# Optimization experiments

Measured on AMD Instinct MI355X. Metric: run time of the kernel, lower is better.

## Reference

```python
import jax, jax.numpy as jnp
import numpy as np

TAW = 0.02

def setup_inputs() -> dict:
    key = jax.random.key(0)
    k1, k2 = jax.random.split(key)
    query = jax.random.normal(k1, (8, 2048, 1024), dtype=jnp.float32)
    memory = jax.random.normal(k2, (8, 2048, 1024), dtype=jnp.float32)
    return {"query": query, "memory": memory}

def reference(query, memory):
    # scores: [B, Lq, Lkv]
    scores = jnp.einsum('bqd,bkd->bqk', query, memory) / TAW
    probs = jax.nn.softmax(scores, axis=-1)
    # out: [B, Lq, D]
    return jnp.einsum('bqk,bkd->bqd', probs, memory)
```

## Files before the change

kernel.cpp:

```cpp
#include <hip/hip_runtime.h>
#include <math.h>


typedef __bf16 bf16x8 __attribute__((ext_vector_type(8)));
typedef float  f32x4  __attribute__((ext_vector_type(4)));
typedef float  f32x16 __attribute__((ext_vector_type(16)));

constexpr int   B_    = 8;
constexpr int   L_    = 2048;
constexpr int   D_    = 1024;
constexpr float SCALE  = 50.0f;
constexpr float MARGIN = 1.2f;
constexpr int   BQ    = 64;
constexpr int   RCAP  = 64;

constexpr size_t WS_T_ELEMS = (size_t)8 * 64 * 2048 * 16;
constexpr size_t WS_NEED    = 2 * WS_T_ELEMS * 2;

static __device__ __forceinline__ unsigned short f2bf(float x) {
    unsigned u = __builtin_bit_cast(unsigned, x);
    u += 0x7FFFu + ((u >> 16) & 1u);
    return (unsigned short)(u >> 16);
}

__global__ __launch_bounds__(256) void convert_k(
    const float* __restrict__ Q, const float* __restrict__ M,
    __bf16* __restrict__ ws)
{
    __shared__ unsigned short lds[64][72];

    const int t   = blockIdx.y;
    const int x   = blockIdx.x;
    const int d0  = x & 15;
    const int r0  = (x >> 4) & 31;
    const int b   = x >> 9;
    const int tid = threadIdx.x;

    const float* src = (t ? M : Q)
                     + ((size_t)b * L_ + (size_t)r0 * 64) * D_ + d0 * 64;

    {
        const int row = tid >> 4;
        const int c4  = tid & 15;
        #pragma unroll
        for (int a = 0; a < 4; ++a) {
            const int rr = a * 16 + row;
            float4 v = *(const float4*)(src + (size_t)rr * D_ + c4 * 4);
            union { unsigned short h[4]; uint2 u; } o;
            o.h[0] = f2bf(v.x); o.h[1] = f2bf(v.y);
            o.h[2] = f2bf(v.z); o.h[3] = f2bf(v.w);
            *(uint2*)&lds[rr][c4 * 4] = o.u;
        }
    }
    __syncthreads();

    {
        const int r    = tid & 63;
        const int d4   = tid >> 6;
        const int dblk = d0 * 4 + d4;
        __bf16* dst = ws + ((size_t)t * 8 + b) * (64ull * 2048 * 16)
                         + ((size_t)dblk * 2048 + (size_t)r0 * 64 + r) * 16;
        uint4 u0 = *(const uint4*)&lds[r][d4 * 16];
        uint4 u1 = *(const uint4*)&lds[r][d4 * 16 + 8];
        ((uint4*)dst)[0] = u0;
        ((uint4*)dst)[1] = u1;
    }
}

__global__ __launch_bounds__(512, 2) void attn_main(
    const float* __restrict__ Q, const float* __restrict__ M,
    const __bf16* __restrict__ ws, float* __restrict__ Out)
{
    __shared__ float wmax[8][BQ];
    __shared__ float rm_s[BQ], thr_s[BQ];
    __shared__ int   rowcnt[BQ];
    __shared__ int   rowlist[BQ][RCAP];
    __shared__ float rowval[BQ][RCAP];

    const int b    = blockIdx.x & 7;
    const int qt   = blockIdx.x >> 3;
    const int q0   = qt * BQ;
    const int tid  = threadIdx.x;
    const int w    = tid >> 6;
    const int lane = tid & 63;
    const int ln31 = lane & 31;
    const int h2   = lane >> 5;

    const __bf16* qws = ws + (size_t)b * (64ull * 2048 * 16);
    const __bf16* mws = ws + ((size_t)8 + b) * (64ull * 2048 * 16);
    const float*  Qb  = Q + ((size_t)b * L_ + q0) * D_;
    const float*  Mb  = M + (size_t)b * L_ * D_;

    if (tid < BQ) { rm_s[tid] = -INFINITY; rowcnt[tid] = 0; }
    __syncthreads();

    constexpr size_t DSTR = 2048 * 16;

    #pragma unroll 1
    for (int kt = 0; kt < 2; ++kt) {
        const int nb = kt * 1024 + w * 128;

        f32x16 acc[2][4];
        #pragma unroll
        for (int i = 0; i < 2; ++i)
            #pragma unroll
            for (int j = 0; j < 4; ++j)
                #pragma unroll
                for (int e = 0; e < 16; ++e) acc[i][j][e] = 0.f;

        const __bf16* qpb = qws + ((size_t)(q0 + ln31)) * 16 + h2 * 8;
        const __bf16* mpb = mws + ((size_t)(nb + ln31)) * 16 + h2 * 8;

        bf16x8 aA0, aA1, bA0, bA1, bA2, bA3;
        bf16x8 aB0, aB1, bB0, bB1, bB2, bB3;

#define LOADSET(s, dblk_) do {                                             \
        const __bf16* qp_##s = qpb + (size_t)(dblk_) * DSTR;               \
        const __bf16* mp_##s = mpb + (size_t)(dblk_) * DSTR;               \
        a##s##0 = *(const bf16x8*)(qp_##s);                                \
        a##s##1 = *(const bf16x8*)(qp_##s + 32 * 16);                      \
        b##s##0 = *(const bf16x8*)(mp_##s);                                \
        b##s##1 = *(const bf16x8*)(mp_##s + 32 * 16);                      \
        b##s##2 = *(const bf16x8*)(mp_##s + 64 * 16);                      \
        b##s##3 = *(const bf16x8*)(mp_##s + 96 * 16);                      \
    } while (0)

#define MFMASET(s) do {                                                    \
        acc[0][0] = __builtin_amdgcn_mfma_f32_32x32x16_bf16(               \
            a##s##0, b##s##0, acc[0][0], 0, 0, 0);                         \
        acc[0][1] = __builtin_amdgcn_mfma_f32_32x32x16_bf16(               \
            a##s##0, b##s##1, acc[0][1], 0, 0, 0);                         \
        acc[0][2] = __builtin_amdgcn_mfma_f32_32x32x16_bf16(               \
            a##s##0, b##s##2, acc[0][2], 0, 0, 0);                         \
        acc[0][3] = __builtin_amdgcn_mfma_f32_32x32x16_bf16(               \
            a##s##0, b##s##3, acc[0][3], 0, 0, 0);                         \
        acc[1][0] = __builtin_amdgcn_mfma_f32_32x32x16_bf16(               \
            a##s##1, b##s##0, acc[1][0], 0, 0, 0);                         \
        acc[1][1] = __builtin_amdgcn_mfma_f32_32x32x16_bf16(               \
            a##s##1, b##s##1, acc[1][1], 0, 0, 0);                         \
        acc[1][2] = __builtin_amdgcn_mfma_f32_32x32x16_bf16(               \
            a##s##1, b##s##2, acc[1][2], 0, 0, 0);                         \
        acc[1][3] = __builtin_amdgcn_mfma_f32_32x32x16_bf16(               \
            a##s##1, b##s##3, acc[1][3], 0, 0, 0);                         \
    } while (0)

        LOADSET(A, 0);
        #pragma unroll 1
        for (int d = 0; d < 62; d += 2) {
            LOADSET(B, d + 1);
            MFMASET(A);
            LOADSET(A, d + 2);
            MFMASET(B);
        }
        LOADSET(B, 63);
        MFMASET(A);
        MFMASET(B);

#undef LOADSET
#undef MFMASET

        float lm[2][16];
        #pragma unroll
        for (int i = 0; i < 2; ++i)
            #pragma unroll
            for (int g = 0; g < 16; ++g)
                lm[i][g] = fmaxf(fmaxf(acc[i][0][g], acc[i][1][g]),
                                 fmaxf(acc[i][2][g], acc[i][3][g]));
        #pragma unroll
        for (int off = 1; off <= 16; off <<= 1)
            #pragma unroll
            for (int i = 0; i < 2; ++i)
                #pragma unroll
                for (int g = 0; g < 16; ++g)
                    lm[i][g] = fmaxf(lm[i][g], __shfl_xor(lm[i][g], off, 64));
        if (ln31 == 0) {
            #pragma unroll
            for (int i = 0; i < 2; ++i)
                #pragma unroll
                for (int g = 0; g < 16; ++g)
                    wmax[w][i * 32 + (g & 3) + 8 * (g >> 2) + 4 * h2] = lm[i][g];
        }
        __syncthreads();
        if (tid < BQ) {
            float m = wmax[0][tid];
            #pragma unroll
            for (int ww = 1; ww < 8; ++ww) m = fmaxf(m, wmax[ww][tid]);
            m = fmaxf(m, rm_s[tid]);
            rm_s[tid] = m;
            thr_s[tid] = m - MARGIN;
        }
        __syncthreads();

        #pragma unroll
        for (int i = 0; i < 2; ++i)
            #pragma unroll
            for (int g = 0; g < 16; ++g) {
                const int rl = i * 32 + (g & 3) + 8 * (g >> 2) + 4 * h2;
                const float thr = thr_s[rl];
                #pragma unroll
                for (int j = 0; j < 4; ++j)
                    if (acc[i][j][g] > thr) {
                        int t = atomicAdd(&rowcnt[rl], 1);
                        if (t < RCAP) {
                            rowlist[rl][t] = nb + j * 32 + ln31;
                            rowval[rl][t]  = acc[i][j][g];
                        }
                    }
            }
    }
    __syncthreads();

    #pragma unroll 1
    for (int r = w; r < BQ; r += 8) {
        const int c = min(rowcnt[r], RCAP);
        const float thrf = rm_s[r] - MARGIN;
        #pragma unroll 1
        for (int t = 0; t < c; ++t) {
            const float av = rowval[r][t];
            if (av > thrf) {
                const int k = rowlist[r][t];
                const f32x4* qp = (const f32x4*)(Qb + (size_t)r * D_);
                const f32x4* mp = (const f32x4*)(Mb + (size_t)k * D_);
                float dot = 0.f;
                #pragma unroll
                for (int c4 = 0; c4 < 4; ++c4) {
                    f32x4 x = qp[lane + 64 * c4];
                    f32x4 y = mp[lane + 64 * c4];
                    dot += x[0]*y[0] + x[1]*y[1] + x[2]*y[2] + x[3]*y[3];
                }
                #pragma unroll
                for (int off = 32; off >= 1; off >>= 1)
                    dot += __shfl_xor(dot, off, 64);
                if (lane == 0) rowval[r][t] = dot;
            } else if (lane == 0) rowval[r][t] = -1e30f;
        }
    }
    __syncthreads();

    #pragma unroll 1
    for (int r = w; r < BQ; r += 8) {
        const int c = min(rowcnt[r], RCAP);
        float mstar = -1e30f;
        for (int t = 0; t < c; ++t) mstar = fmaxf(mstar, rowval[r][t]);
        float denom = 0.f;
        f32x4 o[4];
        #pragma unroll
        for (int c4 = 0; c4 < 4; ++c4) o[c4] = (f32x4){0.f, 0.f, 0.f, 0.f};
        #pragma unroll 1
        for (int t = 0; t < c; ++t) {
            const float wgt = __expf(SCALE * (rowval[r][t] - mstar));
            if (wgt > 1e-22f) {
                denom += wgt;
                const f32x4* mp = (const f32x4*)(Mb + (size_t)rowlist[r][t] * D_);
                #pragma unroll
                for (int c4 = 0; c4 < 4; ++c4)
                    o[c4] += mp[lane + 64 * c4] * wgt;
            }
        }
        const float inv = 1.f / denom;
        f32x4* op = (f32x4*)(Out + ((size_t)b * L_ + q0 + r) * D_);
        #pragma unroll
        for (int c4 = 0; c4 < 4; ++c4) op[lane + 64 * c4] = o[c4] * inv;
    }
}

constexpr int   FB_BKV  = 256;
constexpr int   FB_NKT  = L_ / FB_BKV;
constexpr int   FB_BD   = 32;
constexpr int   FB_NDC  = D_ / FB_BD;
constexpr int   FB_STR  = FB_BD + 8;
constexpr int   FB_CAP  = 2048;

__global__ __launch_bounds__(256) void attn_fb(
    const float* __restrict__ Q, const float* __restrict__ M,
    float* __restrict__ Out)
{
    __shared__ __bf16 qs[BQ * FB_STR];
    __shared__ __bf16 ms[FB_BKV * FB_STR];
    __shared__ float  wmax[4][BQ];
    __shared__ float  rowmax_s[BQ];
    __shared__ int    cnt_s;
    __shared__ int    list_s[FB_CAP];
    __shared__ float  elist_s[FB_CAP];

    const int b    = blockIdx.x & 7;
    const int qt   = blockIdx.x >> 3;
    const int q0   = qt * BQ;
    const int tid  = threadIdx.x;
    const int w    = tid >> 6;
    const int lane = tid & 63;
    const int ln15 = lane & 15;
    const int quad = lane >> 4;

    const float* Qb = Q + ((size_t)b * L_ + q0) * D_;
    const float* Mb = M + (size_t)b * L_ * D_;

    float rm[4][4];
    #pragma unroll
    for (int i = 0; i < 4; ++i)
        #pragma unroll
        for (int r = 0; r < 4; ++r) rm[i][r] = -INFINITY;

    #pragma unroll 1
    for (int pass = 0; pass < 2; ++pass) {
        #pragma unroll 1
        for (int kt = 0; kt < FB_NKT; ++kt) {
            f32x4 acc[4][4];
            #pragma unroll
            for (int i = 0; i < 4; ++i)
                #pragma unroll
                for (int j = 0; j < 4; ++j)
                    acc[i][j] = (f32x4){0.f, 0.f, 0.f, 0.f};
            const float* Mt = Mb + (size_t)(kt * FB_BKV) * D_;
            #pragma unroll 1
            for (int dc = 0; dc < FB_NDC; ++dc) {
                const int d0 = dc * FB_BD;
                __syncthreads();
                #pragma unroll
                for (int i = 0; i < 2; ++i) {
                    int f4 = tid + i * 256, row = f4 >> 3, c = f4 & 7;
                    float4 v = *(const float4*)(Qb + row * D_ + d0 + c * 4);
                    union { unsigned short h[4]; uint2 u; } t;
                    t.h[0] = f2bf(v.x); t.h[1] = f2bf(v.y);
                    t.h[2] = f2bf(v.z); t.h[3] = f2bf(v.w);
                    *(uint2*)(qs + row * FB_STR + c * 4) = t.u;
                }
                #pragma unroll
                for (int i = 0; i < 8; ++i) {
                    int f4 = tid + i * 256, row = f4 >> 3, c = f4 & 7;
                    float4 v = *(const float4*)(Mt + row * D_ + d0 + c * 4);
                    union { unsigned short h[4]; uint2 u; } t;
                    t.h[0] = f2bf(v.x); t.h[1] = f2bf(v.y);
                    t.h[2] = f2bf(v.z); t.h[3] = f2bf(v.w);
                    *(uint2*)(ms + row * FB_STR + c * 4) = t.u;
                }
                __syncthreads();
                bf16x8 afr[4], bfr[4];
                #pragma unroll
                for (int i = 0; i < 4; ++i)
                    afr[i] = *(const bf16x8*)(qs + (i * 16 + ln15) * FB_STR + quad * 8);
                #pragma unroll
                for (int j = 0; j < 4; ++j)
                    bfr[j] = *(const bf16x8*)(ms + (w * 64 + j * 16 + ln15) * FB_STR + quad * 8);
                #pragma unroll
                for (int i = 0; i < 4; ++i)
                    #pragma unroll
                    for (int j = 0; j < 4; ++j)
                        acc[i][j] = __builtin_amdgcn_mfma_f32_16x16x32_bf16(
                            afr[i], bfr[j], acc[i][j], 0, 0, 0);
            }
            if (pass == 0) {
                #pragma unroll
                for (int i = 0; i < 4; ++i)
                    #pragma unroll
                    for (int r = 0; r < 4; ++r) {
                        float m0 = fmaxf(fmaxf(acc[i][0][r], acc[i][1][r]),
                                         fmaxf(acc[i][2][r], acc[i][3][r]));
                        rm[i][r] = fmaxf(rm[i][r], m0);
                    }
            } else {
                #pragma unroll
                for (int i = 0; i < 4; ++i)
                    #pragma unroll
                    for (int j = 0; j < 4; ++j)
                        #pragma unroll
                        for (int r = 0; r < 4; ++r)
                            if (acc[i][j][r] > rm[i][r]) {
                                int idx = atomicAdd(&cnt_s, 1);
                                if (idx < FB_CAP)
                                    list_s[idx] = ((i * 16 + quad * 4 + r) << 16) |
                                                  (kt * FB_BKV + w * 64 + j * 16 + ln15);
                            }
            }
        }
        if (pass == 0) {
            #pragma unroll
            for (int i = 0; i < 4; ++i)
                #pragma unroll
                for (int r = 0; r < 4; ++r) {
                    float v = rm[i][r];
                    v = fmaxf(v, __shfl_xor(v, 1, 64));
                    v = fmaxf(v, __shfl_xor(v, 2, 64));
                    v = fmaxf(v, __shfl_xor(v, 4, 64));
                    v = fmaxf(v, __shfl_xor(v, 8, 64));
                    rm[i][r] = v;
                }
            if (ln15 == 0) {
                #pragma unroll
                for (int i = 0; i < 4; ++i)
                    #pragma unroll
                    for (int r = 0; r < 4; ++r)
                        wmax[w][i * 16 + quad * 4 + r] = rm[i][r];
            }
            __syncthreads();
            if (tid < BQ)
                rowmax_s[tid] = fmaxf(fmaxf(wmax[0][tid], wmax[1][tid]),
                                      fmaxf(wmax[2][tid], wmax[3][tid]));
            if (tid == 0) cnt_s = 0;
            __syncthreads();
            #pragma unroll
            for (int i = 0; i < 4; ++i)
                #pragma unroll
                for (int r = 0; r < 4; ++r)
                    rm[i][r] = rowmax_s[i * 16 + quad * 4 + r] - MARGIN;
        }
    }
    __syncthreads();
    const int n = min(cnt_s, FB_CAP);
    #pragma unroll 1
    for (int s = w; s < n; s += 4) {
        int e = list_s[s];
        int q = e >> 16, k = e & 0xFFFF;
        const float4* qp = (const float4*)(Qb + q * D_);
        const float4* mp = (const float4*)(Mb + (size_t)k * D_);
        float dot = 0.f;
        #pragma unroll
        for (int c = 0; c < 4; ++c) {
            float4 x = qp[lane + 64 * c];
            float4 y = mp[lane + 64 * c];
            dot += x.x * y.x + x.y * y.y + x.z * y.z + x.w * y.w;
        }
        #pragma unroll
        for (int off = 32; off >= 1; off >>= 1)
            dot += __shfl_xor(dot, off, 64);
        if (lane == 0) elist_s[s] = dot;
    }
    __syncthreads();
    #pragma unroll 1
    for (int r = w; r < BQ; r += 4) {
        float mstar = -INFINITY;
        for (int s = 0; s < n; ++s)
            if ((list_s[s] >> 16) == r) mstar = fmaxf(mstar, elist_s[s]);
        float denom = 0.f;
        f32x4 o[4];
        #pragma unroll
        for (int c = 0; c < 4; ++c) o[c] = (f32x4){0.f, 0.f, 0.f, 0.f};
        for (int s = 0; s < n; ++s) {
            if ((list_s[s] >> 16) != r) continue;
            float wgt = __expf(SCALE * (elist_s[s] - mstar));
            denom += wgt;
            const f32x4* mp = (const f32x4*)(Mb + (size_t)(list_s[s] & 0xFFFF) * D_);
            #pragma unroll
            for (int c = 0; c < 4; ++c) o[c] += mp[lane + 64 * c] * wgt;
        }
        const float inv = 1.f / denom;
        f32x4* op = (f32x4*)(Out + ((size_t)b * L_ + q0 + r) * D_);
        #pragma unroll
        for (int c = 0; c < 4; ++c) op[lane + 64 * c] = o[c] * inv;
    }
}

extern "C" void kernel_launch(void* const* d_in, const int* in_sizes, int n_in,
                              void* d_out, int out_size, void* d_ws, size_t ws_size,
                              hipStream_t stream)
{
    const float* Q = (const float*)d_in[0];
    const float* M = (const float*)d_in[1];
    float* Out = (float*)d_out;

    if (ws_size >= WS_NEED) {
        convert_k<<<dim3(4096, 2), 256, 0, stream>>>(Q, M, (__bf16*)d_ws);
        attn_main<<<dim3(256), 512, 0, stream>>>(Q, M, (const __bf16*)d_ws, Out);
    } else {
        attn_fb<<<dim3(256), 256, 0, stream>>>(Q, M, Out);
    }
}
```

Baseline: 278.5 us.

## Shrink per-wave key tile to 64 and deepen load pipeline to four stages

Each wave now covers 64 key columns per pass instead of 128, and the pass count over the key dimension rises from 2 to 4. The MFMA inner loop becomes a 4-deep rotating register prefetch with wrap-around indexing, so loads are issued further ahead of use. This cuts accumulator registers, which may raise occupancy and hide memory latency better. In exchange the Q tile is reloaded twice as often, there are more block-level syncs and threshold passes, and the wrap-around prefetch issues a few redundant loads.

New measurement: 328.4 us. +17.9%, slower.

```diff
diff --git a/kernel.cpp b/kernel.cpp
--- a/kernel.cpp
+++ b/kernel.cpp
@@ -96,23 +96,26 @@
 
     constexpr size_t DSTR = 2048 * 16;
 
-    #pragma unroll 1
-    for (int kt = 0; kt < 2; ++kt) {
-        const int nb = kt * 1024 + w * 128;
-
-        f32x16 acc[2][4];
+    const __bf16* qpb = qws + ((size_t)(q0 + ln31)) * 16 + h2 * 8;
+
+    #pragma unroll 1
+    for (int kt = 0; kt < 4; ++kt) {
+        const int nb = kt * 512 + w * 64;
+
+        f32x16 acc[2][2];
         #pragma unroll
         for (int i = 0; i < 2; ++i)
             #pragma unroll
-            for (int j = 0; j < 4; ++j)
+            for (int j = 0; j < 2; ++j)
                 #pragma unroll
                 for (int e = 0; e < 16; ++e) acc[i][j][e] = 0.f;
 
-        const __bf16* qpb = qws + ((size_t)(q0 + ln31)) * 16 + h2 * 8;
         const __bf16* mpb = mws + ((size_t)(nb + ln31)) * 16 + h2 * 8;
 
-        bf16x8 aA0, aA1, bA0, bA1, bA2, bA3;
-        bf16x8 aB0, aB1, bB0, bB1, bB2, bB3;
+        bf16x8 aA0, aA1, bA0, bA1;
+        bf16x8 aB0, aB1, bB0, bB1;
+        bf16x8 aC0, aC1, bC0, bC1;
+        bf16x8 aD0, aD1, bD0, bD1;
 
 #define LOADSET(s, dblk_) do {                                             \
         const __bf16* qp_##s = qpb + (size_t)(dblk_) * DSTR;               \
@@ -121,8 +124,6 @@
         a##s##1 = *(const bf16x8*)(qp_##s + 32 * 16);                      \
         b##s##0 = *(const bf16x8*)(mp_##s);                                \
         b##s##1 = *(const bf16x8*)(mp_##s + 32 * 16);                      \
-        b##s##2 = *(const bf16x8*)(mp_##s + 64 * 16);                      \
-        b##s##3 = *(const bf16x8*)(mp_##s + 96 * 16);                      \
     } while (0)
 
 #define MFMASET(s) do {                                                    \
@@ -130,31 +131,26 @@
             a##s##0, b##s##0, acc[0][0], 0, 0, 0);                         \
         acc[0][1] = __builtin_amdgcn_mfma_f32_32x32x16_bf16(               \
             a##s##0, b##s##1, acc[0][1], 0, 0, 0);                         \
-        acc[0][2] = __builtin_amdgcn_mfma_f32_32x32x16_bf16(               \
-            a##s##0, b##s##2, acc[0][2], 0, 0, 0);                         \
-        acc[0][3] = __builtin_amdgcn_mfma_f32_32x32x16_bf16(               \
-            a##s##0, b##s##3, acc[0][3], 0, 0, 0);                         \
         acc[1][0] = __builtin_amdgcn_mfma_f32_32x32x16_bf16(               \
             a##s##1, b##s##0, acc[1][0], 0, 0, 0);                         \
         acc[1][1] = __builtin_amdgcn_mfma_f32_32x32x16_bf16(               \
             a##s##1, b##s##1, acc[1][1], 0, 0, 0);                         \
-        acc[1][2] = __builtin_amdgcn_mfma_f32_32x32x16_bf16(               \
-            a##s##1, b##s##2, acc[1][2], 0, 0, 0);                         \
-        acc[1][3] = __builtin_amdgcn_mfma_f32_32x32x16_bf16(               \
-            a##s##1, b##s##3, acc[1][3], 0, 0, 0);                         \
     } while (0)
 
         LOADSET(A, 0);
+        LOADSET(B, 1);
+        LOADSET(C, 2);
         #pragma unroll 1
-        for (int d = 0; d < 62; d += 2) {
-            LOADSET(B, d + 1);
+        for (int d = 0; d < 64; d += 4) {
+            LOADSET(D, (d + 3) & 63);
             MFMASET(A);
-            LOADSET(A, d + 2);
+            LOADSET(A, (d + 4) & 63);
             MFMASET(B);
-        }
-        LOADSET(B, 63);
-        MFMASET(A);
-        MFMASET(B);
+            LOADSET(B, (d + 5) & 63);
+            MFMASET(C);
+            LOADSET(C, (d + 6) & 63);
+            MFMASET(D);
+        }
 
 #undef LOADSET
 #undef MFMASET
@@ -164,8 +160,7 @@
         for (int i = 0; i < 2; ++i)
             #pragma unroll
             for (int g = 0; g < 16; ++g)
-                lm[i][g] = fmaxf(fmaxf(acc[i][0][g], acc[i][1][g]),
-                                 fmaxf(acc[i][2][g], acc[i][3][g]));
+                lm[i][g] = fmaxf(acc[i][0][g], acc[i][1][g]);
         #pragma unroll
         for (int off = 1; off <= 16; off <<= 1)
             #pragma unroll
@@ -198,7 +193,7 @@
                 const int rl = i * 32 + (g & 3) + 8 * (g >> 2) + 4 * h2;
                 const float thr = thr_s[rl];
                 #pragma unroll
-                for (int j = 0; j < 4; ++j)
+                for (int j = 0; j < 2; ++j)
                     if (acc[i][j][g] > thr) {
                         int t = atomicAdd(&rowcnt[rl], 1);
                         if (t < RCAP) {
```

## Stage memory tiles into LDS via async global_load_lds with triple buffering

Applied to the files above, without the earlier changes.

The score GEMM loop now streams the memory operand through a per-wave triple-buffered LDS staging area using direct global-to-LDS loads, then reads fragments from LDS. Query fragments still come straight from global memory. Explicit vmcnt/lgkmcnt waits schedule loads three chunks ahead of the MFMAs, to hide global latency better than the previous register double-buffering. It adds about 104 KB of LDS per block, which may lower occupancy below the two-blocks launch bound. The hand-written waitcnt counts are fragile, and a dummy LDS buffer absorbs the out-of-range tail loads.

Result: slower. 288.2 us (+3.5%).

```diff
diff --git a/kernel.cpp b/kernel.cpp
--- a/kernel.cpp
+++ b/kernel.cpp
@@ -53,7 +53,6 @@
         }
     }
     __syncthreads();
-
     {
         const int r    = tid & 63;
         const int d4   = tid >> 6;
@@ -67,6 +66,64 @@
     }
 }
 
+constexpr size_t DSTR = 2048 * 16;
+constexpr int    CHW  = 2048;
+
+#define GLL16(srcp, dstp)                                                   \
+    __builtin_amdgcn_global_load_lds(                                       \
+        (const __attribute__((address_space(1))) void*)(srcp),              \
+        (__attribute__((address_space(3))) void*)(dstp), 16, 0, 0)
+
+#define STAGE4(srcp, dstp) do {                                             \
+        GLL16((srcp),         (dstp));                                      \
+        GLL16((srcp) +  512,  (dstp) +  512);                               \
+        GLL16((srcp) + 1024,  (dstp) + 1024);                               \
+        GLL16((srcp) + 1536,  (dstp) + 1536);                               \
+    } while (0)
+
+#define DSREAD4(s, rp) do {                                                 \
+        s##0 = *(const bf16x8*)((rp));                                      \
+        s##1 = *(const bf16x8*)((rp) +  512);                               \
+        s##2 = *(const bf16x8*)((rp) + 1024);                               \
+        s##3 = *(const bf16x8*)((rp) + 1536);                               \
+    } while (0)
+
+#define MFMASET(bs, qs) do {                                                \
+        acc[0][0] = __builtin_amdgcn_mfma_f32_32x32x16_bf16(                \
+            qs##0, bs##0, acc[0][0], 0, 0, 0);                              \
+        acc[0][1] = __builtin_amdgcn_mfma_f32_32x32x16_bf16(                \
+            qs##0, bs##1, acc[0][1], 0, 0, 0);                              \
+        acc[0][2] = __builtin_amdgcn_mfma_f32_32x32x16_bf16(                \
+            qs##0, bs##2, acc[0][2], 0, 0, 0);                              \
+        acc[0][3] = __builtin_amdgcn_mfma_f32_32x32x16_bf16(                \
+            qs##0, bs##3, acc[0][3], 0, 0, 0);                              \
+        acc[1][0] = __builtin_amdgcn_mfma_f32_32x32x16_bf16(                \
+            qs##1, bs##0, acc[1][0], 0, 0, 0);                              \
+        acc[1][1] = __builtin_amdgcn_mfma_f32_32x32x16_bf16(                \
+            qs##1, bs##1, acc[1][1], 0, 0, 0);                              \
+        acc[1][2] = __builtin_amdgcn_mfma_f32_32x32x16_bf16(                \
+            qs##1, bs##2, acc[1][2], 0, 0, 0);                              \
+        acc[1][3] = __builtin_amdgcn_mfma_f32_32x32x16_bf16(                \
+            qs##1, bs##3, acc[1][3], 0, 0, 0);                              \
+    } while (0)
+
+#define PHASE(dd, bc, qc, bn, qn) do {                                      \
+        asm volatile("s_waitcnt vmcnt(6)" ::: "memory");                    \
+        { const __bf16* rp = buf0 + (size_t)(((dd) + 1) % 3) * CHW + roff;  \
+          DSREAD4(bn, rp); }                                                \
+        asm volatile("s_waitcnt lgkmcnt(4)" ::: "memory");                  \
+        { const int c1 = (dd) + 1 <= 63 ? (dd) + 1 : 63;                    \
+          const __bf16* qp = qbase + (size_t)c1 * DSTR;                     \
+          qn##0 = *(const bf16x8*)(qp);                                     \
+          qn##1 = *(const bf16x8*)(qp + 512); }                             \
+        { const int c3 = (dd) + 3;                                          \
+          const __bf16* sp = mlane + (size_t)(c3 <= 63 ? c3 : 63) * DSTR;   \
+          __bf16* sd = (c3 <= 63) ? (buf0 + (size_t)(c3 % 3) * CHW)         \
+                                  : dummy_s;                                \
+          STAGE4(sp, sd); }                                                 \
+        MFMASET(bc, qc);                                                    \
+    } while (0)
+
 __global__ __launch_bounds__(512, 2) void attn_main(
     const float* __restrict__ Q, const float* __restrict__ M,
     const __bf16* __restrict__ ws, float* __restrict__ Out)
@@ -76,6 +133,8 @@
     __shared__ int   rowcnt[BQ];
     __shared__ int   rowlist[BQ][RCAP];
     __shared__ float rowval[BQ][RCAP];
+    __shared__ __attribute__((aligned(16))) __bf16 stg[8][3][CHW];
+    __shared__ __attribute__((aligned(16))) __bf16 dummy_s[CHW];
 
     const int b    = blockIdx.x & 7;
     const int qt   = blockIdx.x >> 3;
@@ -94,7 +153,9 @@
     if (tid < BQ) { rm_s[tid] = -INFINITY; rowcnt[tid] = 0; }
     __syncthreads();
 
-    constexpr size_t DSTR = 2048 * 16;
+    __bf16* buf0 = &stg[w][0][0];
+    const int roff = ln31 * 16 + h2 * 8;
+    const __bf16* qbase = qws + ((size_t)(q0 + ln31)) * 16 + h2 * 8;
 
     #pragma unroll 1
     for (int kt = 0; kt < 2; ++kt) {
@@ -108,56 +169,33 @@
                 #pragma unroll
                 for (int e = 0; e < 16; ++e) acc[i][j][e] = 0.f;
 
-        const __bf16* qpb = qws + ((size_t)(q0 + ln31)) * 16 + h2 * 8;
-        const __bf16* mpb = mws + ((size_t)(nb + ln31)) * 16 + h2 * 8;
-
-        bf16x8 aA0, aA1, bA0, bA1, bA2, bA3;
-        bf16x8 aB0, aB1, bB0, bB1, bB2, bB3;
-
-#define LOADSET(s, dblk_) do {                                             \
-        const __bf16* qp_##s = qpb + (size_t)(dblk_) * DSTR;               \
-        const __bf16* mp_##s = mpb + (size_t)(dblk_) * DSTR;               \
-        a##s##0 = *(const bf16x8*)(qp_##s);                                \
-        a##s##1 = *(const bf16x8*)(qp_##s + 32 * 16);                      \
-        b##s##0 = *(const bf16x8*)(mp_##s);                                \
-        b##s##1 = *(const bf16x8*)(mp_##s + 32 * 16);                      \
-        b##s##2 = *(const bf16x8*)(mp_##s + 64 * 16);                      \
-        b##s##3 = *(const bf16x8*)(mp_##s + 96 * 16);                      \
-    } while (0)
-
-#define MFMASET(s) do {                                                    \
-        acc[0][0] = __builtin_amdgcn_mfma_f32_32x32x16_bf16(               \
-            a##s##0, b##s##0, acc[0][0], 0, 0, 0);                         \
-        acc[0][1] = __builtin_amdgcn_mfma_f32_32x32x16_bf16(               \
-            a##s##0, b##s##1, acc[0][1], 0, 0, 0);                         \
-        acc[0][2] = __builtin_amdgcn_mfma_f32_32x32x16_bf16(               \
-            a##s##0, b##s##2, acc[0][2], 0, 0, 0);                         \
-        acc[0][3] = __builtin_amdgcn_mfma_f32_32x32x16_bf16(               \
-            a##s##0, b##s##3, acc[0][3], 0, 0, 0);                         \
-        acc[1][0] = __builtin_amdgcn_mfma_f32_32x32x16_bf16(               \
-            a##s##1, b##s##0, acc[1][0], 0, 0, 0);                         \
-        acc[1][1] = __builtin_amdgcn_mfma_f32_32x32x16_bf16(               \
-            a##s##1, b##s##1, acc[1][1], 0, 0, 0);                         \
-        acc[1][2] = __builtin_amdgcn_mfma_f32_32x32x16_bf16(               \
-            a##s##1, b##s##2, acc[1][2], 0, 0, 0);                         \
-        acc[1][3] = __builtin_amdgcn_mfma_f32_32x32x16_bf16(               \
-            a##s##1, b##s##3, acc[1][3], 0, 0, 0);                         \
-    } while (0)
-
-        LOADSET(A, 0);
+        const __bf16* mlane = mws + (size_t)nb * 16 + (size_t)lane * 8;
+
+        bf16x8 qA0, qA1, qB0, qB1;
+        bf16x8 bA0, bA1, bA2, bA3, bB0, bB1, bB2, bB3;
+
+        qA0 = *(const bf16x8*)(qbase);
+        qA1 = *(const bf16x8*)(qbase + 512);
+        STAGE4(mlane,            buf0);
+        STAGE4(mlane + DSTR,     buf0 + CHW);
+        STAGE4(mlane + 2 * DSTR, buf0 + 2 * CHW);
+        asm volatile("s_waitcnt vmcnt(8)" ::: "memory");
+        DSREAD4(bA, buf0 + roff);
+
+        asm volatile("s_waitcnt vmcnt(4)" ::: "memory");
+        DSREAD4(bB, buf0 + CHW + roff);
+        asm volatile("s_waitcnt lgkmcnt(4)" ::: "memory");
+        qB0 = *(const bf16x8*)(qbase + DSTR);
+        qB1 = *(const bf16x8*)(qbase + DSTR + 512);
+        STAGE4(mlane + 3 * DSTR, buf0);
+        MFMASET(bA, qA);
+
         #pragma unroll 1
-        for (int d = 0; d < 62; d += 2) {
-            LOADSET(B, d + 1);
-            MFMASET(A);
-            LOADSET(A, d + 2);
-            MFMASET(B);
-        }
-        LOADSET(B, 63);
-        MFMASET(A);
-        MFMASET(B);
-
-#undef LOADSET
-#undef MFMASET
+        for (int d = 1; d < 63; d += 2) {
+            PHASE(d,     bB, qB, bA, qA);
+            PHASE(d + 1, bA, qA, bB, qB);
+        }
+        PHASE(63, bB, qB, bA, qA);
 
         float lm[2][16];
         #pragma unroll
```
